# Performance work log

Hardware: AMD Instinct MI355X
Metric: run time of the kernel (lower is better)

Reference implementation:

```python
import jax, jax.numpy as jnp
import numpy as np

B, S, D, MEM, STRIDE = 8, 8192, 128, 128, 64

def setup_inputs() -> dict:
    key = jax.random.key(0)
    ks = jax.random.split(key, 6)
    scale = 0.01  # matches nn.init.normal_(w, 0.0, 0.01)
    x = jax.random.normal(ks[0], (B, S, D), dtype=jnp.float32)
    Wq = scale * jax.random.normal(ks[1], (D, D), dtype=jnp.float32)
    Wk = scale * jax.random.normal(ks[2], (D, D), dtype=jnp.float32)
    Wv = scale * jax.random.normal(ks[3], (MEM, D), dtype=jnp.float32)
    Wg_w = jnp.zeros((1, D), dtype=jnp.float32)       # W_g weight init zeros
    Wg_b = jnp.full((1,), -2.0, dtype=jnp.float32)    # W_g bias init -2.0
    Wout = scale * jax.random.normal(ks[4], (D, MEM), dtype=jnp.float32)
    return {"x": x, "Wq": Wq, "Wk": Wk, "Wv": Wv, "Wg_w": Wg_w, "Wg_b": Wg_b, "Wout": Wout}

def reference(x, Wq, Wk, Wv, Wg_w, Wg_b, Wout):
    b, s, d = x.shape
    nC = s // STRIDE  # S assumed divisible by stride
    q = x @ Wq.T                                  # [B,S,D]
    k = x @ Wk.T                                  # [B,S,D]
    v = x @ Wv.T                                  # [B,S,MEM]
    g = jax.nn.sigmoid(x @ Wg_w.T + Wg_b)         # [B,S,1]
    # chunk: leading scan axis nC
    qc = q.reshape(b, nC, STRIDE, d).transpose(1, 0, 2, 3)
    kc = k.reshape(b, nC, STRIDE, d).transpose(1, 0, 2, 3)
    vc = v.reshape(b, nC, STRIDE, MEM).transpose(1, 0, 2, 3)
    gc = g.reshape(b, nC, STRIDE, 1).transpose(1, 0, 2, 3)

    def step(M, chunk):
        qch, kch, vch, gch = chunk
        reads = jnp.einsum('bsd,bdm->bsm', qch, M)              # read before write
        write = jnp.einsum('bsd,bsm->bdm', kch * gch, vch)      # gated outer-product
        avg_gate = gch.mean(axis=1, keepdims=True)              # [B,1,1]
        M_new = (1.0 - avg_gate) * M + write
        return M_new, reads

    M0 = jnp.zeros((b, d, MEM), dtype=x.dtype)
    _, reads = jax.lax.scan(step, M0, (qc, kc, vc, gc))         # [nC,B,STRIDE,MEM]
    out = reads.transpose(1, 0, 2, 3).reshape(b, s, MEM)
    return out @ Wout.T                                         # [B,S,D]
```

## Files before the change

### kernel.cpp

```cpp
#include <hip/hip_runtime.h>

#define Bn 8
#define Sn 8192
#define Dn 128
#define NCn 128

typedef _Float16 f16;
typedef f16 f16x2 __attribute__((ext_vector_type(2)));
typedef f16 f16x4 __attribute__((ext_vector_type(4)));
typedef float f32x4 __attribute__((ext_vector_type(4)));

static __device__ __forceinline__ f32x4 mfma16(f16x4 a, f16x4 b, f32x4 c) {
  return __builtin_amdgcn_mfma_f32_16x16x16f16(a, b, c, 0, 0, 0);
}


static __device__ __forceinline__ void stage_T136(const float* __restrict__ src,
                                                  f16* __restrict__ dst, int tid) {
#pragma unroll
  for (int ii = 0; ii < 4; ++ii) {
    int id = ii * 256 + tid;
    int r4 = id >> 5, c4 = id & 31;
    float4 row[4];
#pragma unroll
    for (int i = 0; i < 4; ++i)
      row[i] = *(const float4*)(src + (r4 * 4 + i) * 128 + c4 * 4);
#pragma unroll
    for (int j = 0; j < 4; ++j) {
      f16x4 col = {(f16)(((const float*)&row[0])[j]), (f16)(((const float*)&row[1])[j]),
                   (f16)(((const float*)&row[2])[j]), (f16)(((const float*)&row[3])[j])};
      *(f16x4*)&dst[(c4 * 4 + j) * 136 + r4 * 4] = col;
    }
  }
}

__global__ __launch_bounds__(256) void k_prep(
    const float* __restrict__ Wq, const float* __restrict__ Wk,
    const float* __restrict__ Wv, const float* __restrict__ Wout,
    f16* __restrict__ Amat, f16* __restrict__ r2) {
  __shared__ __align__(16) f16 L[128 * 136];
  __shared__ __align__(16) f16 R[128 * 136];
  const int tid = threadIdx.x;
  if (blockIdx.x == 0) {
    stage_T136(Wq, L, tid);
    stage_T136(Wk, R, tid);
  } else {
    int r = tid >> 1, h = tid & 1;
#pragma unroll
    for (int i = 0; i < 16; ++i) {
      float4 v = *(const float4*)(Wout + r * 128 + h * 64 + i * 4);
      f16x4 o = {(f16)v.x, (f16)v.y, (f16)v.z, (f16)v.w};
      *(f16x4*)&L[r * 136 + h * 64 + i * 4] = o;
    }
    stage_T136(Wv, R, tid);
  }
  __syncthreads();
  const int w = tid >> 6, lane = tid & 63, r16 = lane & 15, g4 = lane >> 4;
  f32x4 acc[2][8] = {};
#pragma unroll
  for (int kk = 0; kk < 8; ++kk) {
    f16x4 af0 = *(f16x4*)&L[((2 * w) * 16 + r16) * 136 + kk * 16 + g4 * 4];
    f16x4 af1 = *(f16x4*)&L[((2 * w + 1) * 16 + r16) * 136 + kk * 16 + g4 * 4];
#pragma unroll
    for (int ct = 0; ct < 8; ++ct) {
      f16x4 bf = *(f16x4*)&R[(ct * 16 + r16) * 136 + kk * 16 + g4 * 4];
      acc[0][ct] = mfma16(af0, bf, acc[0][ct]);
      acc[1][ct] = mfma16(af1, bf, acc[1][ct]);
    }
  }
  f16* dst = (blockIdx.x == 0) ? Amat : r2;
#pragma unroll
  for (int rr = 0; rr < 2; ++rr)
#pragma unroll
    for (int ct = 0; ct < 8; ++ct)
#pragma unroll
      for (int j = 0; j < 4; ++j)
        dst[((2 * w + rr) * 16 + g4 * 4 + j) * 128 + ct * 16 + r16] = (f16)acc[rr][ct][j];
}

__global__ __launch_bounds__(512, 4) void k_phase1(
    const float* __restrict__ x, const float* __restrict__ gw, const float* __restrict__ gb,
    const f16* __restrict__ Amat, const f16* __restrict__ r2,
    f16x4* __restrict__ wtg, float* __restrict__ gavg) {
  __shared__ __align__(16) f16 Xs[64][136];
  __shared__ __align__(16) f16x4 vP[4096];
  __shared__ float gs[64];
  const int blk = blockIdx.x, b = blk >> 7, c = blk & 127;
  const int tid = threadIdx.x;
  {
    int s = tid >> 3, sub = tid & 7;
    const float* xrow = x + ((size_t)b * Sn + (size_t)c * 64 + s) * Dn;
    float gpart = 0.f;
#pragma unroll
    for (int i = 0; i < 4; ++i) {
      int col = sub * 4 + i * 32;
      float4 v = *(const float4*)(xrow + col);
      float4 g = *(const float4*)(gw + col);
      gpart += v.x * g.x + v.y * g.y + v.z * g.z + v.w * g.w;
      f16x4 h = {(f16)v.x, (f16)v.y, (f16)v.z, (f16)v.w};
      *(f16x4*)&Xs[s][col] = h;
    }
    gpart += __shfl_xor(gpart, 1);
    gpart += __shfl_xor(gpart, 2);
    gpart += __shfl_xor(gpart, 4);
    if (sub == 0) gs[s] = 1.f / (1.f + __expf(-(gpart + gb[0])));
  }
  __syncthreads();
  if (tid == 0) {
    float sum = 0.f;
#pragma unroll
    for (int i = 0; i < 64; ++i) sum += gs[i];
    gavg[blk] = sum * (1.f / 64.f);
  }
  const int w = tid >> 6, lane = tid & 63, r16 = lane & 15, g4 = lane >> 4;

  f32x4 uacc[4] = {}, vacc[4] = {};
#pragma unroll
  for (int kk = 0; kk < 8; ++kk) {
    f16x4 bu = *(const f16x4*)&Amat[(w * 16 + r16) * 128 + kk * 16 + g4 * 4];
    f16x4 bv = *(const f16x4*)&r2[(w * 16 + r16) * 128 + kk * 16 + g4 * 4];
#pragma unroll
    for (int mr = 0; mr < 4; ++mr) {
      f16x4 af = *(f16x4*)&Xs[mr * 16 + r16][kk * 16 + g4 * 4];
      uacc[mr] = mfma16(af, bu, uacc[mr]);
      vacc[mr] = mfma16(af, bv, vacc[mr]);
    }
  }
  f16x4 ua[4];
#pragma unroll
  for (int mr = 0; mr < 4; ++mr) {
    float g0 = gs[mr * 16 + g4 * 4 + 0], g1 = gs[mr * 16 + g4 * 4 + 1];
    float g2 = gs[mr * 16 + g4 * 4 + 2], g3 = gs[mr * 16 + g4 * 4 + 3];
    f16x4 uh = {(f16)(uacc[mr][0] * g0), (f16)(uacc[mr][1] * g1),
                (f16)(uacc[mr][2] * g2), (f16)(uacc[mr][3] * g3)};
    ua[mr] = uh;
    f16x4 vh = {(f16)vacc[mr][0], (f16)vacc[mr][1], (f16)vacc[mr][2], (f16)vacc[mr][3]};
    vP[(mr * 8 + w) * 64 + lane] = vh;
  }
  __syncthreads();

  f32x4 z[8] = {};
#pragma unroll
  for (int ks = 0; ks < 4; ++ks)
#pragma unroll
    for (int ct = 0; ct < 8; ++ct)
      z[ct] = mfma16(ua[ks], vP[(ks * 8 + ct) * 64 + lane], z[ct]);

  f16x4* wdst = wtg + (size_t)blk * 4096;
#pragma unroll
  for (int ct = 0; ct < 8; ++ct) {
    f16x4 zh = {(f16)z[ct][0], (f16)z[ct][1], (f16)z[ct][2], (f16)z[ct][3]};
    wdst[(w * 8 + ct) * 64 + lane] = zh;
  }
}

__global__ __launch_bounds__(256) void k_scan(
    const uint* __restrict__ wtg, const float* __restrict__ gavg, uint* __restrict__ mtg) {
  const int blk = blockIdx.x;
  const int b = blk >> 5;
  const int e = (blk & 31) * 256 + threadIdx.x;
  const uint* wp = wtg + (size_t)b * (NCn * 8192) + e;
  uint* mp = mtg + (size_t)b * (NCn * 8192) + e;
  const float* ga = gavg + b * NCn;
  float M0 = 0.f, M1 = 0.f;
  uint ubuf[16];
  float abuf[16];
#pragma unroll
  for (int i = 0; i < 16; ++i) {
    ubuf[i] = wp[(size_t)i * 8192];
    abuf[i] = ga[i];
  }
  for (int g = 0; g < 8; ++g) {
    uint un[16];
    float an[16];
    if (g < 7) {
#pragma unroll
      for (int i = 0; i < 16; ++i) {
        un[i] = wp[(size_t)((g + 1) * 16 + i) * 8192];
        an[i] = ga[(g + 1) * 16 + i];
      }
    }
#pragma unroll
    for (int i = 0; i < 16; ++i) {
      int cc = g * 16 + i;
      f16x2 mv = {(f16)M0, (f16)M1};
      mp[(size_t)cc * 8192] = __builtin_bit_cast(uint, mv);
      f16x2 wv = __builtin_bit_cast(f16x2, ubuf[i]);
      float d = 1.f - abuf[i];
      M0 = d * M0 + (float)wv[0];
      M1 = d * M1 + (float)wv[1];
    }
#pragma unroll
    for (int i = 0; i < 16; ++i) { ubuf[i] = un[i]; abuf[i] = an[i]; }
  }
}

__global__ __launch_bounds__(512, 4) void k_out(
    const float* __restrict__ x, const f16x4* __restrict__ mtg, float* __restrict__ outp) {
  __shared__ __align__(16) f16 Xs[64][136];
  __shared__ __align__(16) f16x4 zP[4096];
  const int blk = blockIdx.x, b = blk >> 7, c = blk & 127;
  const int tid = threadIdx.x;
  {
    int s = tid >> 3, sub = tid & 7;
    const float* xrow = x + ((size_t)b * Sn + (size_t)c * 64 + s) * Dn;
#pragma unroll
    for (int i = 0; i < 4; ++i) {
      int col = sub * 4 + i * 32;
      float4 v = *(const float4*)(xrow + col);
      f16x4 h = {(f16)v.x, (f16)v.y, (f16)v.z, (f16)v.w};
      *(f16x4*)&Xs[s][col] = h;
    }
    const uint4* src = (const uint4*)(mtg + (size_t)blk * 4096);
    uint4* dst = (uint4*)zP;
#pragma unroll
    for (int i = 0; i < 4; ++i) {
      int idx = tid + i * 512;
      dst[idx] = src[idx];
    }
  }
  __syncthreads();
  const int w = tid >> 6, lane = tid & 63, r16 = lane & 15, g4 = lane >> 4;
  const int mr = w & 3, cb = (w >> 2) * 4;
  f32x4 acc[4] = {};
#pragma unroll
  for (int kk = 0; kk < 8; ++kk) {
    f16x4 af = *(f16x4*)&Xs[mr * 16 + r16][kk * 16 + g4 * 4];
#pragma unroll
    for (int t = 0; t < 4; ++t)
      acc[t] = mfma16(af, zP[(kk * 8 + cb + t) * 64 + lane], acc[t]);
  }
  float* obase = outp + ((size_t)b * Sn + (size_t)c * 64 + mr * 16 + g4 * 4) * Dn;
#pragma unroll
  for (int t = 0; t < 4; ++t)
#pragma unroll
    for (int j = 0; j < 4; ++j)
      obase[(size_t)j * Dn + (cb + t) * 16 + r16] = acc[t][j];
}

extern "C" void kernel_launch(void* const* d_in, const int* in_sizes, int n_in,
                              void* d_out, int out_size, void* d_ws, size_t ws_size,
                              hipStream_t stream) {
  const float* x = (const float*)d_in[0];
  const float* Wq = (const float*)d_in[1];
  const float* Wk = (const float*)d_in[2];
  const float* Wv = (const float*)d_in[3];
  const float* gw = (const float*)d_in[4];
  const float* gb = (const float*)d_in[5];
  const float* Wout = (const float*)d_in[6];

  char* ws = (char*)d_ws;
  f16* Amat = (f16*)(ws + 0);
  f16* r2 = (f16*)(ws + 32768);
  float* gavg = (float*)(ws + 65536);
  f16* wtg = (f16*)(ws + 69632);
  f16* mtg = (f16*)(ws + 69632 + 33554432);

  k_prep<<<dim3(2), dim3(256), 0, stream>>>(Wq, Wk, Wv, Wout, Amat, r2);
  k_phase1<<<dim3(Bn * NCn), dim3(512), 0, stream>>>(x, gw, gb, Amat, r2, (f16x4*)wtg, gavg);
  k_scan<<<dim3(256), dim3(256), 0, stream>>>((const uint*)wtg, gavg, (uint*)mtg);
  k_out<<<dim3(Bn * NCn), dim3(512), 0, stream>>>(x, (const f16x4*)mtg, (float*)d_out);
}
```

Baseline: 63.98 us.

## Write only segment checkpoints in scan and reconstruct chunk states in output kernel

The scan now stores the memory state only at every eighth chunk boundary (15 checkpoints per batch) instead of writing the full state for all 128 chunks. The output kernel rebuilds each chunk's state from the previous checkpoint plus up to seven decayed write updates, and the phase1/out grids are remapped so blocks sharing a segment run close together. This removes most of the scan's large state-write traffic and the matching reads, but adds redundant loads and accumulation in k_out, and the rebuilt state is stored in fp16. k_prep is also split across 8 blocks instead of 2 to spread the weight-product work.

```diff
diff --git a/kernel.cpp b/kernel.cpp
--- a/kernel.cpp
+++ b/kernel.cpp
@@ -14,6 +14,8 @@
   return __builtin_amdgcn_mfma_f32_16x16x16f16(a, b, c, 0, 0, 0);
 }
 
+union UU { uint4 u; f16x2 h[4]; };
+
 
 static __device__ __forceinline__ void stage_T136(const float* __restrict__ src,
                                                   f16* __restrict__ dst, int tid) {
@@ -38,44 +40,54 @@
     const float* __restrict__ Wq, const float* __restrict__ Wk,
     const float* __restrict__ Wv, const float* __restrict__ Wout,
     f16* __restrict__ Amat, f16* __restrict__ r2) {
-  __shared__ __align__(16) f16 L[128 * 136];
+  __shared__ __align__(16) f16 Ls[32 * 136];
   __shared__ __align__(16) f16 R[128 * 136];
+  const int blk = blockIdx.x;
+  const int which = blk >> 2, j = blk & 3;
   const int tid = threadIdx.x;
-  if (blockIdx.x == 0) {
-    stage_T136(Wq, L, tid);
+  if (which == 0) {
+    int kb = tid >> 3, cb = tid & 7;
+    float4 row[4];
+#pragma unroll
+    for (int i = 0; i < 4; ++i)
+      row[i] = *(const float4*)(Wq + (kb * 4 + i) * 128 + j * 32 + cb * 4);
+#pragma unroll
+    for (int jj = 0; jj < 4; ++jj) {
+      f16x4 col = {(f16)(((const float*)&row[0])[jj]), (f16)(((const float*)&row[1])[jj]),
+                   (f16)(((const float*)&row[2])[jj]), (f16)(((const float*)&row[3])[jj])};
+      *(f16x4*)&Ls[(cb * 4 + jj) * 136 + kb * 4] = col;
+    }
     stage_T136(Wk, R, tid);
   } else {
-    int r = tid >> 1, h = tid & 1;
-#pragma unroll
-    for (int i = 0; i < 16; ++i) {
-      float4 v = *(const float4*)(Wout + r * 128 + h * 64 + i * 4);
-      f16x4 o = {(f16)v.x, (f16)v.y, (f16)v.z, (f16)v.w};
-      *(f16x4*)&L[r * 136 + h * 64 + i * 4] = o;
+    int r = tid >> 3, sub = tid & 7;
+#pragma unroll
+    for (int i = 0; i < 4; ++i) {
+      int col = sub * 4 + i * 32;
+      float4 v = *(const float4*)(Wout + (j * 32 + r) * 128 + col);
+      f16x4 h = {(f16)v.x, (f16)v.y, (f16)v.z, (f16)v.w};
+      *(f16x4*)&Ls[r * 136 + col] = h;
     }
     stage_T136(Wv, R, tid);
   }
   __syncthreads();
   const int w = tid >> 6, lane = tid & 63, r16 = lane & 15, g4 = lane >> 4;
-  f32x4 acc[2][8] = {};
+  const int rt = w & 1, cb4 = (w >> 1) * 4;
+  f32x4 acc[4] = {};
 #pragma unroll
   for (int kk = 0; kk < 8; ++kk) {
-    f16x4 af0 = *(f16x4*)&L[((2 * w) * 16 + r16) * 136 + kk * 16 + g4 * 4];
-    f16x4 af1 = *(f16x4*)&L[((2 * w + 1) * 16 + r16) * 136 + kk * 16 + g4 * 4];
-#pragma unroll
-    for (int ct = 0; ct < 8; ++ct) {
-      f16x4 bf = *(f16x4*)&R[(ct * 16 + r16) * 136 + kk * 16 + g4 * 4];
-      acc[0][ct] = mfma16(af0, bf, acc[0][ct]);
-      acc[1][ct] = mfma16(af1, bf, acc[1][ct]);
-    }
-  }
-  f16* dst = (blockIdx.x == 0) ? Amat : r2;
-#pragma unroll
-  for (int rr = 0; rr < 2; ++rr)
-#pragma unroll
-    for (int ct = 0; ct < 8; ++ct)
-#pragma unroll
-      for (int j = 0; j < 4; ++j)
-        dst[((2 * w + rr) * 16 + g4 * 4 + j) * 128 + ct * 16 + r16] = (f16)acc[rr][ct][j];
+    f16x4 af = *(f16x4*)&Ls[(rt * 16 + r16) * 136 + kk * 16 + g4 * 4];
+#pragma unroll
+    for (int t = 0; t < 4; ++t) {
+      f16x4 bf = *(f16x4*)&R[((cb4 + t) * 16 + r16) * 136 + kk * 16 + g4 * 4];
+      acc[t] = mfma16(af, bf, acc[t]);
+    }
+  }
+  f16* dst = which ? r2 : Amat;
+#pragma unroll
+  for (int t = 0; t < 4; ++t)
+#pragma unroll
+    for (int jj = 0; jj < 4; ++jj)
+      dst[(j * 32 + rt * 16 + g4 * 4 + jj) * 128 + (cb4 + t) * 16 + r16] = (f16)acc[t][jj];
 }
 
 __global__ __launch_bounds__(512, 4) void k_phase1(
@@ -85,7 +97,10 @@
   __shared__ __align__(16) f16 Xs[64][136];
   __shared__ __align__(16) f16x4 vP[4096];
   __shared__ float gs[64];
-  const int blk = blockIdx.x, b = blk >> 7, c = blk & 127;
+  const int h = blockIdx.x;
+  const int grp = h & 127, m = h >> 7;
+  const int b = grp >> 4, seg = grp & 15;
+  const int c = seg * 8 + m;
   const int tid = threadIdx.x;
   {
     int s = tid >> 3, sub = tid & 7;
@@ -97,8 +112,8 @@
       float4 v = *(const float4*)(xrow + col);
       float4 g = *(const float4*)(gw + col);
       gpart += v.x * g.x + v.y * g.y + v.z * g.z + v.w * g.w;
-      f16x4 h = {(f16)v.x, (f16)v.y, (f16)v.z, (f16)v.w};
-      *(f16x4*)&Xs[s][col] = h;
+      f16x4 hh = {(f16)v.x, (f16)v.y, (f16)v.z, (f16)v.w};
+      *(f16x4*)&Xs[s][col] = hh;
     }
     gpart += __shfl_xor(gpart, 1);
     gpart += __shfl_xor(gpart, 2);
@@ -110,7 +125,7 @@
     float sum = 0.f;
 #pragma unroll
     for (int i = 0; i < 64; ++i) sum += gs[i];
-    gavg[blk] = sum * (1.f / 64.f);
+    gavg[b * NCn + c] = sum * (1.f / 64.f);
   }
   const int w = tid >> 6, lane = tid & 63, r16 = lane & 15, g4 = lane >> 4;
 
@@ -146,7 +161,7 @@
     for (int ct = 0; ct < 8; ++ct)
       z[ct] = mfma16(ua[ks], vP[(ks * 8 + ct) * 64 + lane], z[ct]);
 
-  f16x4* wdst = wtg + (size_t)blk * 4096;
+  f16x4* wdst = wtg + (size_t)(b * NCn + c) * 4096;
 #pragma unroll
   for (int ct = 0; ct < 8; ++ct) {
     f16x4 zh = {(f16)z[ct][0], (f16)z[ct][1], (f16)z[ct][2], (f16)z[ct][3]};
@@ -155,12 +170,12 @@
 }
 
 __global__ __launch_bounds__(256) void k_scan(
-    const uint* __restrict__ wtg, const float* __restrict__ gavg, uint* __restrict__ mtg) {
+    const uint* __restrict__ wtg, const float* __restrict__ gavg, uint* __restrict__ pbuf) {
   const int blk = blockIdx.x;
   const int b = blk >> 5;
   const int e = (blk & 31) * 256 + threadIdx.x;
   const uint* wp = wtg + (size_t)b * (NCn * 8192) + e;
-  uint* mp = mtg + (size_t)b * (NCn * 8192) + e;
+  uint* pp = pbuf + (size_t)b * (15 * 8192) + e;
   const float* ga = gavg + b * NCn;
   float M0 = 0.f, M1 = 0.f;
   uint ubuf[16];
@@ -183,23 +198,32 @@
 #pragma unroll
     for (int i = 0; i < 16; ++i) {
       int cc = g * 16 + i;
-      f16x2 mv = {(f16)M0, (f16)M1};
-      mp[(size_t)cc * 8192] = __builtin_bit_cast(uint, mv);
       f16x2 wv = __builtin_bit_cast(f16x2, ubuf[i]);
-      float d = 1.f - abuf[i];
-      M0 = d * M0 + (float)wv[0];
-      M1 = d * M1 + (float)wv[1];
-    }
-#pragma unroll
-    for (int i = 0; i < 16; ++i) { ubuf[i] = un[i]; abuf[i] = an[i]; }
+      float dd = 1.f - abuf[i];
+      M0 = dd * M0 + (float)wv[0];
+      M1 = dd * M1 + (float)wv[1];
+      if ((cc & 7) == 7 && cc < 120) {
+        f16x2 mv = {(f16)M0, (f16)M1};
+        pp[(size_t)(cc >> 3) * 8192] = __builtin_bit_cast(uint, mv);
+      }
+    }
+    if (g < 7) {
+#pragma unroll
+      for (int i = 0; i < 16; ++i) { ubuf[i] = un[i]; abuf[i] = an[i]; }
+    }
   }
 }
 
 __global__ __launch_bounds__(512, 4) void k_out(
-    const float* __restrict__ x, const f16x4* __restrict__ mtg, float* __restrict__ outp) {
+    const float* __restrict__ x, const uint4* __restrict__ wtg4,
+    const uint4* __restrict__ pbuf4, const float* __restrict__ gavg,
+    float* __restrict__ outp) {
   __shared__ __align__(16) f16 Xs[64][136];
   __shared__ __align__(16) f16x4 zP[4096];
-  const int blk = blockIdx.x, b = blk >> 7, c = blk & 127;
+  const int h = blockIdx.x;
+  const int grp = h & 127, m = h >> 7;
+  const int b = grp >> 4, seg = grp & 15;
+  const int c = seg * 8 + m;
   const int tid = threadIdx.x;
   {
     int s = tid >> 3, sub = tid & 7;
@@ -208,16 +232,52 @@
     for (int i = 0; i < 4; ++i) {
       int col = sub * 4 + i * 32;
       float4 v = *(const float4*)(xrow + col);
-      f16x4 h = {(f16)v.x, (f16)v.y, (f16)v.z, (f16)v.w};
-      *(f16x4*)&Xs[s][col] = h;
-    }
-    const uint4* src = (const uint4*)(mtg + (size_t)blk * 4096);
-    uint4* dst = (uint4*)zP;
-#pragma unroll
-    for (int i = 0; i < 4; ++i) {
-      int idx = tid + i * 512;
-      dst[idx] = src[idx];
-    }
+      f16x4 hh = {(f16)v.x, (f16)v.y, (f16)v.z, (f16)v.w};
+      *(f16x4*)&Xs[s][col] = hh;
+    }
+  }
+  float d[8], sfac[8];
+#pragma unroll
+  for (int t = 0; t < 8; ++t)
+    d[t] = (t < m) ? (1.f - gavg[b * NCn + seg * 8 + t]) : 1.f;
+  sfac[7] = 1.f;
+#pragma unroll
+  for (int t = 6; t >= 0; --t) sfac[t] = sfac[t + 1] * d[t + 1];
+  const float sP = sfac[0] * d[0];
+
+  const uint4* Zp[8];
+#pragma unroll
+  for (int t = 0; t < 8; ++t)
+    Zp[t] = wtg4 + (size_t)(b * NCn + seg * 8 + t) * 2048;
+  const uint4* Pp = pbuf4 + (size_t)(b * 15 + (seg > 0 ? seg - 1 : 0)) * 2048;
+
+#pragma unroll
+  for (int i = 0; i < 4; ++i) {
+    int idx = tid + i * 512;
+    float a8[8] = {0.f, 0.f, 0.f, 0.f, 0.f, 0.f, 0.f, 0.f};
+    if (seg > 0) {
+      UU z; z.u = Pp[idx];
+#pragma unroll
+      for (int q = 0; q < 4; ++q) {
+        a8[2 * q] += sP * (float)z.h[q][0];
+        a8[2 * q + 1] += sP * (float)z.h[q][1];
+      }
+    }
+#pragma unroll
+    for (int t = 0; t < 8; ++t)
+      if (t < m) {
+        UU z; z.u = Zp[t][idx];
+#pragma unroll
+        for (int q = 0; q < 4; ++q) {
+          a8[2 * q] += sfac[t] * (float)z.h[q][0];
+          a8[2 * q + 1] += sfac[t] * (float)z.h[q][1];
+        }
+      }
+    UU o;
+#pragma unroll
+    for (int q = 0; q < 4; ++q)
+      o.h[q] = (f16x2){(f16)a8[2 * q], (f16)a8[2 * q + 1]};
+    ((uint4*)zP)[idx] = o.u;
   }
   __syncthreads();
   const int w = tid >> 6, lane = tid & 63, r16 = lane & 15, g4 = lane >> 4;
@@ -254,10 +314,11 @@
   f16* r2 = (f16*)(ws + 32768);
   float* gavg = (float*)(ws + 65536);
   f16* wtg = (f16*)(ws + 69632);
-  f16* mtg = (f16*)(ws + 69632 + 33554432);
-
-  k_prep<<<dim3(2), dim3(256), 0, stream>>>(Wq, Wk, Wv, Wout, Amat, r2);
+  f16* pbuf = (f16*)(ws + 69632 + 33554432);
+
+  k_prep<<<dim3(8), dim3(256), 0, stream>>>(Wq, Wk, Wv, Wout, Amat, r2);
   k_phase1<<<dim3(Bn * NCn), dim3(512), 0, stream>>>(x, gw, gb, Amat, r2, (f16x4*)wtg, gavg);
-  k_scan<<<dim3(256), dim3(256), 0, stream>>>((const uint*)wtg, gavg, (uint*)mtg);
-  k_out<<<dim3(Bn * NCn), dim3(512), 0, stream>>>(x, (const f16x4*)mtg, (float*)d_out);
-}
+  k_scan<<<dim3(256), dim3(256), 0, stream>>>((const uint*)wtg, gavg, (uint*)pbuf);
+  k_out<<<dim3(Bn * NCn), dim3(512), 0, stream>>>(x, (const uint4*)wtg, (const uint4*)pbuf,
+                                                  gavg, (float*)d_out);
+}
```

Result: no change. 65.21 us (+1.9%).
